# Kernel optimization log

Hardware: AMD Instinct MI355X
Metric: run time of the kernel (lower is better)

## Reference

```python
import jax, jax.numpy as jnp
import numpy as np

EPS = 1e-8  # EPSILON in original repo (sharpen denom); cosine eps matches torch default 1e-8
MAX_SHIFT = 1
M_FEAT = 128


def _lstm_cell(x, h, c, W_ih, W_hh, b_ih, b_hh):
    gates = x @ W_ih.T + b_ih + h @ W_hh.T + b_hh
    i, f, g, o = jnp.split(gates, 4, axis=1)
    c_new = jax.nn.sigmoid(f) * c + jax.nn.sigmoid(i) * jnp.tanh(g)
    h_new = jax.nn.sigmoid(o) * jnp.tanh(c_new)
    return h_new, c_new


def _content_address(bank, k, b):
    # torch cosine_similarity over dim 2: dot / max(|m||k|, eps)
    dot = jnp.einsum('bnm,bm->bn', bank, k)
    denom = jnp.maximum(jnp.linalg.norm(bank, axis=2) * jnp.linalg.norm(k, axis=1, keepdims=True), 1e-8)
    return jax.nn.softmax(b * dot / denom, axis=1)


def _shift(w, s):
    # circular unroll then valid cross-correlation with per-batch kernel s [B, 2*MAX_SHIFT+1]
    wp = jnp.concatenate([w[:, -MAX_SHIFT:], w, w[:, :MAX_SHIFT]], axis=1)
    N = w.shape[1]
    taps = 2 * MAX_SHIFT + 1
    return sum(s[:, i:i + 1] * wp[:, i:i + N] for i in range(taps))


def _sharpen(w, r):
    wr = w ** r
    return wr / (wr.sum(axis=1, keepdims=True) + EPS)


def _move(bank, w_prev, k, b, g, s, r):
    w = _content_address(bank, k, b)
    w = w + (1.0 - g) * w_prev  # faithful: w_c is NOT scaled by g in the source
    w = _shift(w, s)
    return _sharpen(w, r)


def _split_read(p):
    M = M_FEAT
    k = p[:, :M]
    b = jax.nn.softplus(p[:, M:M + 1])
    g = jax.nn.sigmoid(p[:, M + 1:M + 2])
    s = jax.nn.softmax(p[:, M + 2:M + 5], axis=1)
    r = 1.0 + jax.nn.softplus(p[:, M + 5:M + 6])
    return k, b, g, s, r


def _split_write(p):
    M = M_FEAT
    k, b, g, s, r = _split_read(p[:, :M + 6])
    e = jax.nn.sigmoid(p[:, M + 6:M + 6 + M])
    a = p[:, M + 6 + M:M + 6 + 2 * M]
    return k, b, g, s, r, e, a


def setup_inputs() -> dict:
    key = jax.random.key(0)
    ks = jax.random.split(key, 16)
    B, E, H, N, M, O = 64, 256, 512, 4096, 128, 256
    rd_out, wr_out = M + 2 * MAX_SHIFT + 4, 3 * M + 2 * MAX_SHIFT + 4
    sc = 0.05
    return {
        'x': jax.random.normal(ks[0], (B, E), jnp.float32),
        'h_prev': jax.random.normal(ks[1], (B, H), jnp.float32),
        'c_prev': jax.random.normal(ks[2], (B, H), jnp.float32),
        'bank': jax.random.normal(ks[3], (B, N, M), jnp.float32) * 0.1,
        'read_w_prev': jnp.zeros((3, B, N), jnp.float32),
        'write_w_prev': jnp.zeros((3, B, N), jnp.float32),
        'W_ih': jax.random.normal(ks[4], (4 * H, E), jnp.float32) * sc,
        'W_hh': jax.random.normal(ks[5], (4 * H, H), jnp.float32) * sc,
        'b_ih': jax.random.normal(ks[6], (4 * H,), jnp.float32) * sc,
        'b_hh': jax.random.normal(ks[7], (4 * H,), jnp.float32) * sc,
        'read_W': jax.random.normal(ks[8], (3, rd_out, H), jnp.float32) * sc,
        'read_b': jax.random.normal(ks[9], (3, rd_out), jnp.float32) * sc,
        'write_W': jax.random.normal(ks[10], (3, wr_out, H), jnp.float32) * sc,
        'write_b': jax.random.normal(ks[11], (3, wr_out), jnp.float32) * sc,
        'out_W': jax.random.normal(ks[12], (O, 3 * M + H), jnp.float32) * sc,
        'out_b': jax.random.normal(ks[13], (O,), jnp.float32) * sc,
    }


def reference(x, h_prev, c_prev, bank, read_w_prev, write_w_prev,
              W_ih, W_hh, b_ih, b_hh, read_W, read_b, write_W, write_b,
              out_W, out_b):
    h, c = _lstm_cell(x, h_prev, c_prev, W_ih, W_hh, b_ih, b_hh)
    reads = []
    for i in range(3):  # head_num=3, structurally distinct params per head
        # write head: update bank
        pw = h @ write_W[i].T + write_b[i]
        k, b, g, s, r, e, a = _split_write(pw)
        ww = _move(bank, write_w_prev[i], k, b, g, s, r)
        bank = bank * (1.0 - ww[:, :, None] * e[:, None, :]) + ww[:, :, None] * a[:, None, :]
        # read head: read from updated bank
        pr = h @ read_W[i].T + read_b[i]
        k, b, g, s, r = _split_read(pr)
        wr = _move(bank, read_w_prev[i], k, b, g, s, r)
        reads.append(jnp.einsum('bn,bnm->bm', wr, bank))
    out = jnp.concatenate(reads + [h], axis=1) @ out_W.T + out_b
    return out
```

## Files before the change

kernel.cpp:

```cpp
#include <hip/hip_runtime.h>
#include <math.h>

namespace {

constexpr int kB = 64;
constexpr int kN = 4096;
constexpr int kM = 128;
constexpr int kH = 512;
constexpr int kE = 256;
constexpr int kO = 256;
constexpr int kGates = 4 * kH;
constexpr int kCatW = 3 * kM + kH;
constexpr int kPRow = 1600;
constexpr int kWN = kB * kN;
constexpr float kLog2e = 1.4426950408889634f;

__device__ __forceinline__ float sigm_(float x) { return 1.f / (1.f + expf(-x)); }
__device__ __forceinline__ float softplus_(float x) { return x > 20.f ? x : log1pf(expf(x)); }

__global__ __launch_bounds__(256) void gates_gemm(const float* __restrict__ x,
                                                  const float* __restrict__ W_ih,
                                                  const float* __restrict__ h_prev,
                                                  const float* __restrict__ W_hh,
                                                  float* __restrict__ gates,
                                                  const float* __restrict__ out_b,
                                                  float* __restrict__ out,
                                                  float* __restrict__ cat) {
  if (blockIdx.x == 32) {
    const int tid = threadIdx.x;
    for (int i = tid; i < kB * kO; i += 256) out[i] = out_b[i & (kO - 1)];
    for (int i = tid; i < kB * 384; i += 256) cat[(i / 384) * kCatW + (i % 384)] = 0.f;
    return;
  }
  __shared__ float As[64][68];
  __shared__ float Ws[64][68];
  const int tid = threadIdx.x;
  const int j0 = blockIdx.x * 64;
  const int b0 = (tid & 15) * 4;
  const int j4 = (tid >> 4) * 4;
  float acc[4][4] = {};
  for (int kc = 0; kc < 12; kc++) {
    const bool isx = kc < 4;
    const float* A = isx ? x : h_prev;
    const float* W = isx ? W_ih : W_hh;
    const int lda = isx ? kE : kH;
    const int k0 = (isx ? kc : (kc - 4)) * 64;
    __syncthreads();
#pragma unroll
    for (int i = 0; i < 4; i++) {
      int idx = tid + i * 256;
      int bb = idx >> 4;
      int kk = (idx & 15) * 4;
      float4 v = *(const float4*)(A + (size_t)bb * lda + k0 + kk);
      As[kk][bb] = v.x; As[kk + 1][bb] = v.y; As[kk + 2][bb] = v.z; As[kk + 3][bb] = v.w;
      float4 w = *(const float4*)(W + (size_t)(j0 + bb) * lda + k0 + kk);
      Ws[kk][bb] = w.x; Ws[kk + 1][bb] = w.y; Ws[kk + 2][bb] = w.z; Ws[kk + 3][bb] = w.w;
    }
    __syncthreads();
#pragma unroll 2
    for (int k = 0; k < 64; k++) {
      float4 av = *(const float4*)&As[k][b0];
      float4 wv = *(const float4*)&Ws[k][j4];
      float aa[4] = {av.x, av.y, av.z, av.w};
      float ww[4] = {wv.x, wv.y, wv.z, wv.w};
#pragma unroll
      for (int ii = 0; ii < 4; ii++)
#pragma unroll
        for (int jj = 0; jj < 4; jj++) acc[ii][jj] += aa[ii] * ww[jj];
    }
  }
#pragma unroll
  for (int ii = 0; ii < 4; ii++) {
    float4 st = make_float4(acc[ii][0], acc[ii][1], acc[ii][2], acc[ii][3]);
    *(float4*)&gates[(size_t)(b0 + ii) * kGates + j0 + j4] = st;
  }
}

__global__ __launch_bounds__(256) void lstm_nl(const float* __restrict__ gates,
                                               const float* __restrict__ b_ih,
                                               const float* __restrict__ b_hh,
                                               const float* __restrict__ c_prev,
                                               float* __restrict__ cat) {
  int idx = blockIdx.x * 256 + threadIdx.x;
  if (idx >= kB * kH) return;
  int b = idx >> 9;
  int hh = idx & (kH - 1);
  const float* g = gates + (size_t)b * kGates;
  float i_ = g[hh]          + b_ih[hh]          + b_hh[hh];
  float f_ = g[kH + hh]     + b_ih[kH + hh]     + b_hh[kH + hh];
  float g_ = g[2 * kH + hh] + b_ih[2 * kH + hh] + b_hh[2 * kH + hh];
  float o_ = g[3 * kH + hh] + b_ih[3 * kH + hh] + b_hh[3 * kH + hh];
  float c = sigm_(f_) * c_prev[idx] + sigm_(i_) * tanhf(g_);
  cat[(size_t)b * kCatW + 3 * kM + hh] = sigm_(o_) * tanhf(c);
}

__global__ __launch_bounds__(256) void proj_gemm(const float* __restrict__ cat,
                                                 const float* __restrict__ write_W,
                                                 const float* __restrict__ read_W,
                                                 float* __restrict__ praw) {
  __shared__ float As[64][68];
  __shared__ float Ws[64][68];
  const float* A = cat + 3 * kM;
  const int tid = threadIdx.x;
  const int j0 = blockIdx.x * 64;
  const int b0 = (tid & 15) * 4;
  const int j4 = (tid >> 4) * 4;
  float acc[4][4] = {};
  for (int kc = 0; kc < 8; kc++) {
    const int k0 = kc * 64;
    __syncthreads();
#pragma unroll
    for (int i = 0; i < 4; i++) {
      int idx = tid + i * 256;
      int bb = idx >> 4;
      int kk = (idx & 15) * 4;
      float4 v = *(const float4*)(A + (size_t)bb * kCatW + k0 + kk);
      As[kk][bb] = v.x; As[kk + 1][bb] = v.y; As[kk + 2][bb] = v.z; As[kk + 3][bb] = v.w;
      int j = j0 + bb;
      float4 w = make_float4(0.f, 0.f, 0.f, 0.f);
      if (j < 1170)      w = *(const float4*)(write_W + (size_t)j * kH + k0 + kk);
      else if (j < 1572) w = *(const float4*)(read_W + (size_t)(j - 1170) * kH + k0 + kk);
      Ws[kk][bb] = w.x; Ws[kk + 1][bb] = w.y; Ws[kk + 2][bb] = w.z; Ws[kk + 3][bb] = w.w;
    }
    __syncthreads();
#pragma unroll 2
    for (int k = 0; k < 64; k++) {
      float4 av = *(const float4*)&As[k][b0];
      float4 wv = *(const float4*)&Ws[k][j4];
      float aa[4] = {av.x, av.y, av.z, av.w};
      float ww[4] = {wv.x, wv.y, wv.z, wv.w};
#pragma unroll
      for (int ii = 0; ii < 4; ii++)
#pragma unroll
        for (int jj = 0; jj < 4; jj++) acc[ii][jj] += aa[ii] * ww[jj];
    }
  }
  if (j0 + j4 < 1572) {
#pragma unroll
    for (int ii = 0; ii < 4; ii++) {
      float4 st = make_float4(acc[ii][0], acc[ii][1], acc[ii][2], acc[ii][3]);
      *(float4*)&praw[(size_t)(b0 + ii) * kPRow + j0 + j4] = st;
    }
  }
}

__global__ __launch_bounds__(128) void split_params(const float* __restrict__ praw,
                                                    const float* __restrict__ write_b,
                                                    const float* __restrict__ read_b,
                                                    float* __restrict__ kwb, float* __restrict__ krb,
                                                    float* __restrict__ evb, float* __restrict__ avb,
                                                    float* __restrict__ scal,
                                                    float* __restrict__ sdot) {
  const int b = blockIdx.x;
  const int m = threadIdx.x;
  __shared__ float red[2];
  for (int i = 0; i < 3; i++) {
    const float* p = praw + (size_t)b * kPRow + i * 390;
    const float* wb = write_b + i * 390;
    float kv = p[m] + wb[m];
    kwb[((size_t)i * kB + b) * kM + m] = kv;
    evb[((size_t)i * kB + b) * kM + m] = sigm_(p[134 + m] + wb[134 + m]);
    avb[((size_t)i * kB + b) * kM + m] = p[262 + m] + wb[262 + m];
    float sq = kv * kv;
#pragma unroll
    for (int mm = 1; mm < 64; mm <<= 1) sq += __shfl_xor(sq, mm, 64);
    __syncthreads();
    if ((m & 63) == 0) red[m >> 6] = sq;
    __syncthreads();
    if (m == 0) {
      float* s = scal + ((size_t)i * kB + b) * 8;
      s[0] = softplus_(p[128] + wb[128]);
      s[1] = sigm_(p[129] + wb[129]);
      s[2] = 1.f + softplus_(p[133] + wb[133]);
      float x0 = p[130] + wb[130], x1 = p[131] + wb[131], x2 = p[132] + wb[132];
      float mx = fmaxf(x0, fmaxf(x1, x2));
// ... 19 lines not shown
      float* s = scal + ((size_t)(3 + i) * kB + b) * 8;
      s[0] = softplus_(p[128] + rb[128]);
      s[1] = sigm_(p[129] + rb[129]);
      s[2] = 1.f + softplus_(p[133] + rb[133]);
      float x0 = p[130] + rb[130], x1 = p[131] + rb[131], x2 = p[132] + rb[132];
      float mx = fmaxf(x0, fmaxf(x1, x2));
      float e0 = expf(x0 - mx), e1 = expf(x1 - mx), e2 = expf(x2 - mx);
      float si = 1.f / (e0 + e1 + e2);
      s[3] = e0 * si; s[4] = e1 * si; s[5] = e2 * si;
      s[6] = sqrtf(red[0] + red[1]);
    }
    __syncthreads();
  }
  __syncthreads();
  if (m < 64) {
    const float* a0 = avb + ((size_t)0 * kB + b) * kM;
    const float* a2 = avb + ((size_t)2 * kB + b) * kM;
    const float* u[5] = {a0, a0, a0, a2, a2};
    const float* v[5] = {krb + ((size_t)0 * kB + b) * kM,
                         kwb + ((size_t)1 * kB + b) * kM,
                         a0,
                         krb + ((size_t)2 * kB + b) * kM,
                         a2};
#pragma unroll
    for (int d = 0; d < 5; d++) {
      float s = u[d][m] * v[d][m] + u[d][m + 64] * v[d][m + 64];
#pragma unroll
      for (int mm = 1; mm < 64; mm <<= 1) s += __shfl_xor(s, mm, 64);
      if (m == 0) sdot[b * 8 + d] = s;
    }
  }
}

__global__ __launch_bounds__(256, 4) void passA_k(const float* __restrict__ bank,
                                                  const float* __restrict__ kwb,
                                                  const float* __restrict__ krb,
                                                  const float* __restrict__ evb,
                                                  const float* __restrict__ avb,
                                                  float* __restrict__ mA) {
  const int b = blockIdx.y, chunk = blockIdx.x;
  const int tid = threadIdx.x;
  const int lane = tid & 63, wv = tid >> 6, sub = lane >> 4, lm = lane & 15;
  const int m8 = lm * 8;
  float kw0r[8], kr0r[8], kw1r[8], a0r[8], e0r[8];
#pragma unroll
  for (int t = 0; t < 8; t++) {
    kw0r[t] = kwb[((size_t)0 * kB + b) * kM + m8 + t];
    kr0r[t] = krb[((size_t)0 * kB + b) * kM + m8 + t];
    kw1r[t] = kwb[((size_t)1 * kB + b) * kM + m8 + t];
    a0r[t]  = avb[((size_t)0 * kB + b) * kM + m8 + t];
    e0r[t]  = evb[((size_t)0 * kB + b) * kM + m8 + t];
  }
  const size_t bbase = (size_t)b * kN * kM;
  const size_t brow = (size_t)b * kN;
  const int row0 = chunk * 256 + wv * 4 + sub;
  const float* rp = bank + bbase + (size_t)row0 * kM + m8;
  float4 c0 = *(const float4*)rp;
  float4 c1 = *(const float4*)(rp + 4);
  for (int it = 0; it < 16; it++) {
    float v[8] = {c0.x, c0.y, c0.z, c0.w, c1.x, c1.y, c1.z, c1.w};
    if (it < 15) {
      const float* np = bank + bbase + (size_t)(row0 + (it + 1) * 16) * kM + m8;
      c0 = *(const float4*)np;
      c1 = *(const float4*)(np + 4);
    }
    const int row = row0 + it * 16;
    float s[10] = {};
#pragma unroll
    for (int t = 0; t < 8; t++) {
      float be = v[t] * e0r[t];
      s[0] += v[t] * kw0r[t];
      s[1] += v[t] * v[t];
      s[2] += v[t] * kr0r[t];
      s[3] += be * kr0r[t];
      s[4] += v[t] * kw1r[t];
      s[5] += be * kw1r[t];
      s[6] += be * v[t];
      s[7] += be * be;
      s[8] += v[t] * a0r[t];
      s[9] += be * a0r[t];
    }
#pragma unroll
    for (int m = 1; m < 16; m <<= 1)
#pragma unroll
      for (int k = 0; k < 10; k++) s[k] += __shfl_xor(s[k], m, 64);
    if (lm == 0) {
#pragma unroll
      for (int k = 0; k < 10; k++) mA[(size_t)k * kWN + brow + row] = s[k];
    }
  }
}

__device__ void addr_core4(int tid, float* loc, const float* sc, const float* __restrict__ wp,
                           float* wb, float* red) {
  const float g = sc[1], r = sc[2];
  const float s0 = sc[3], s1c = sc[4], s2 = sc[5];
  const int lane = tid & 63, wid = tid >> 6;
  __syncthreads();
  float mx = fmaxf(fmaxf(loc[0], loc[1]), fmaxf(loc[2], loc[3]));
#pragma unroll
  for (int m = 1; m < 64; m <<= 1) mx = fmaxf(mx, __shfl_xor(mx, m, 64));
  if (lane == 0) red[wid] = mx;
  __syncthreads();
  mx = red[0];
#pragma unroll
  for (int k = 1; k < 16; k++) mx = fmaxf(mx, red[k]);
  float sum = 0.f;
#pragma unroll
  for (int i = 0; i < 4; i++) { loc[i] = exp2f((loc[i] - mx) * kLog2e); sum += loc[i]; }
#pragma unroll
  for (int m = 1; m < 64; m <<= 1) sum += __shfl_xor(sum, m, 64);
  __syncthreads();
  if (lane == 0) red[wid] = sum;
  __syncthreads();
  sum = red[0];
#pragma unroll
  for (int k = 1; k < 16; k++) sum += red[k];
  const float inv = 1.f / sum;
  const float omg = 1.f - g;
#pragma unroll
  for (int i = 0; i < 4; i++) {
    int n = tid + i * 1024;
    wb[n] = loc[i] * inv + omg * wp[n];
  }
  __syncthreads();
  float ssum = 0.f;
#pragma unroll
  for (int i = 0; i < 4; i++) {
    int n = tid + i * 1024;
    float sh = s0 * wb[(n + kN - 1) & (kN - 1)] + s1c * wb[n] + s2 * wb[(n + 1) & (kN - 1)];
    float y = (sh > 0.f) ? exp2f(r * log2f(sh)) : 0.f;
    loc[i] = y;
    ssum += y;
  }
#pragma unroll
  for (int m = 1; m < 64; m <<= 1) ssum += __shfl_xor(ssum, m, 64);
  __syncthreads();
  if (lane == 0) red[wid] = ssum;
  __syncthreads();
  ssum = red[0];
#pragma unroll
  for (int k = 1; k < 16; k++) ssum += red[k];
  const float invs = 1.f / (ssum + 1e-8f);
#pragma unroll
  for (int i = 0; i < 4; i++) loc[i] *= invs;
  __syncthreads();
}

__global__ __launch_bounds__(1024) void a12_k(const float* __restrict__ mA,
                                              const float* __restrict__ scal,
                                              const float* __restrict__ sdot,
                                              const float* __restrict__ read_w_prev,
                                              const float* __restrict__ write_w_prev,
                                              float* __restrict__ wwv,
                                              float* __restrict__ wrv) {
  const int b = blockIdx.x;
  const int tid = threadIdx.x;
  __shared__ float wb[kN];
  __shared__ float red[16];
  const size_t brow = (size_t)b * kN;
  float loc[4], w0r[4], q1r[4];
  {
    const float* sc = scal + ((size_t)0 * kB + b) * 8;
    const float beta = sc[0], kn = sc[6];
#pragma unroll
    for (int i = 0; i < 4; i++) {
      size_t idx = brow + tid + i * 1024;
      float d = mA[0 * (size_t)kWN + idx];
      float q = mA[1 * (size_t)kWN + idx];
      loc[i] = beta * d / fmaxf(sqrtf(fmaxf(q, 0.f)) * kn, 1e-8f);
    }
    addr_core4(tid, loc, sc, write_w_prev + brow, wb, red);
#pragma unroll
    for (int i = 0; i < 4; i++) { wwv[brow + tid + i * 1024] = loc[i]; w0r[i] = loc[i]; }
  }
  {
    const float* sc = scal + ((size_t)3 * kB + b) * 8;
    const float beta = sc[0], kn = sc[6];
    const float sa0kr0 = sdot[b * 8 + 0], sa0a0 = sdot[b * 8 + 2];
#pragma unroll
    for (int i = 0; i < 4; i++) {
      size_t idx = brow + tid + i * 1024;
      float w0 = w0r[i], w0q = w0 * w0;
      float q1 = mA[1 * (size_t)kWN + idx]
               - 2.f * w0 * mA[6 * (size_t)kWN + idx]
               + w0q * mA[7 * (size_t)kWN + idx]
               + 2.f * w0 * mA[8 * (size_t)kWN + idx]
               - 2.f * w0q * mA[9 * (size_t)kWN + idx]
               + w0q * sa0a0;
      q1r[i] = q1;
      float d = mA[2 * (size_t)kWN + idx] - w0 * mA[3 * (size_t)kWN + idx] + w0 * sa0kr0;
      loc[i] = beta * d / fmaxf(sqrtf(fmaxf(q1, 0.f)) * kn, 1e-8f);
    }
    addr_core4(tid, loc, sc, read_w_prev + brow, wb, red);
#pragma unroll
    for (int i = 0; i < 4; i++) wrv[brow + tid + i * 1024] = loc[i];
  }
  {
    const float* sc = scal + ((size_t)1 * kB + b) * 8;
    const float beta = sc[0], kn = sc[6];
    const float sa0kw1 = sdot[b * 8 + 1];
#pragma unroll
    for (int i = 0; i < 4; i++) {
      size_t idx = brow + tid + i * 1024;
      float w0 = w0r[i];
      float d = mA[4 * (size_t)kWN + idx] - w0 * mA[5 * (size_t)kWN + idx] + w0 * sa0kw1;
      loc[i] = beta * d / fmaxf(sqrtf(fmaxf(q1r[i], 0.f)) * kn, 1e-8f);
    }
    addr_core4(tid, loc, sc, write_w_prev + kWN + brow, wb, red);
#pragma unroll
    for (int i = 0; i < 4; i++) wwv[kWN + brow + tid + i * 1024] = loc[i];
  }
}

__global__ __launch_bounds__(256, 4) void passB_k(const float* __restrict__ bank,
                                                  const float* __restrict__ wwv,
                                                  const float* __restrict__ wrv,
                                                  const float* __restrict__ kwb,
                                                  const float* __restrict__ krb,
                                                  const float* __restrict__ evb,
                                                  const float* __restrict__ avb,
                                                  float* __restrict__ cat,
                                                  float* __restrict__ mB) {
  const int b = blockIdx.y, chunk = blockIdx.x;
  const int tid = threadIdx.x;
  const int lane = tid & 63, wv = tid >> 6, sub = lane >> 4, lm = lane & 15;
  const int m8 = lm * 8;
  float e0r[8], a0r[8], e1r[8], a1r[8], kr1r[8], kw2r[8], kr2r[8], e2r[8], a2r[8];
#pragma unroll
  for (int t = 0; t < 8; t++) {
    e0r[t]  = evb[((size_t)0 * kB + b) * kM + m8 + t];
    a0r[t]  = avb[((size_t)0 * kB + b) * kM + m8 + t];
    e1r[t]  = evb[((size_t)1 * kB + b) * kM + m8 + t];
    a1r[t]  = avb[((size_t)1 * kB + b) * kM + m8 + t];
    kr1r[t] = krb[((size_t)1 * kB + b) * kM + m8 + t];
    kw2r[t] = kwb[((size_t)2 * kB + b) * kM + m8 + t];
    kr2r[t] = krb[((size_t)2 * kB + b) * kM + m8 + t];
    e2r[t]  = evb[((size_t)2 * kB + b) * kM + m8 + t];
    a2r[t]  = avb[((size_t)2 * kB + b) * kM + m8 + t];
  }
  float racc[8] = {};
  __shared__ float rlds[kM];
  if (tid < kM) rlds[tid] = 0.f;
  const size_t bbase = (size_t)b * kN * kM;
  const size_t brow = (size_t)b * kN;
  const int row0 = chunk * 256 + wv * 4 + sub;
  const float* rp = bank + bbase + (size_t)row0 * kM + m8;
  float4 c0 = *(const float4*)rp;
  float4 c1 = *(const float4*)(rp + 4);
  float w0p = wwv[brow + row0];
  float w1p = wwv[kWN + brow + row0];
  float wr0p = wrv[brow + row0];
  for (int it = 0; it < 16; it++) {
    float v[8] = {c0.x, c0.y, c0.z, c0.w, c1.x, c1.y, c1.z, c1.w};
    const float w0 = w0p, w1 = w1p, wr0 = wr0p;
    if (it < 15) {
      const int nrow = row0 + (it + 1) * 16;
      const float* np = bank + bbase + (size_t)nrow * kM + m8;
      c0 = *(const float4*)np;
      c1 = *(const float4*)(np + 4);
      w0p = wwv[brow + nrow];
      w1p = wwv[kWN + brow + nrow];
      wr0p = wrv[brow + nrow];
    }
    const int row = row0 + it * 16;
#pragma unroll
    for (int t = 0; t < 8; t++) {
      v[t] += w0 * (a0r[t] - e0r[t] * v[t]);
      racc[t] += wr0 * v[t];
      v[t] += w1 * (a1r[t] - e1r[t] * v[t]);
    }
    float s[9] = {};
#pragma unroll
    for (int t = 0; t < 8; t++) {
      float ve = v[t] * e2r[t];
      s[0] += v[t] * kr1r[t];
      s[1] += v[t] * kw2r[t];
      s[2] += v[t] * v[t];
      s[3] += v[t] * kr2r[t];
      s[4] += ve * kr2r[t];
      s[5] += ve * v[t];
      s[6] += ve * ve;
      s[7] += v[t] * a2r[t];
      s[8] += ve * a2r[t];
    }
#pragma unroll
    for (int m = 1; m < 16; m <<= 1)
#pragma unroll
      for (int k = 0; k < 9; k++) s[k] += __shfl_xor(s[k], m, 64);
    if (lm == 0) {
#pragma unroll
      for (int k = 0; k < 9; k++) mB[(size_t)k * kWN + brow + row] = s[k];
    }
  }
  __syncthreads();
#pragma unroll
  for (int t = 0; t < 8; t++) {
    racc[t] += __shfl_xor(racc[t], 16, 64);
    racc[t] += __shfl_xor(racc[t], 32, 64);
  }
  if (sub == 0) {
#pragma unroll
    for (int t = 0; t < 8; t++) atomicAdd(&rlds[m8 + t], racc[t]);
  }
  __syncthreads();
  if (tid < kM) atomicAdd(&cat[(size_t)b * kCatW + tid], rlds[tid]);
}

__global__ __launch_bounds__(1024) void a34_k(const float* __restrict__ mB,
                                              const float* __restrict__ scal,
                                              const float* __restrict__ sdot,
                                              const float* __restrict__ read_w_prev,
                                              const float* __restrict__ write_w_prev,
                                              float* __restrict__ wwv,
                                              float* __restrict__ wrv) {
  const int b = blockIdx.x;
  const int tid = threadIdx.x;
  __shared__ float wb[kN];
  __shared__ float red[16];
  const size_t brow = (size_t)b * kN;
  float loc[4], w2r[4];
  {
    const float* sc = scal + ((size_t)4 * kB + b) * 8;
    const float beta = sc[0], kn = sc[6];
#pragma unroll
    for (int i = 0; i < 4; i++) {
      size_t idx = brow + tid + i * 1024;
      float d = mB[0 * (size_t)kWN + idx];
      float q = mB[2 * (size_t)kWN + idx];
      loc[i] = beta * d / fmaxf(sqrtf(fmaxf(q, 0.f)) * kn, 1e-8f);
    }
    addr_core4(tid, loc, sc, read_w_prev + kWN + brow, wb, red);
#pragma unroll
    for (int i = 0; i < 4; i++) wrv[kWN + brow + tid + i * 1024] = loc[i];
  }
  {
    const float* sc = scal + ((size_t)2 * kB + b) * 8;
    const float beta = sc[0], kn = sc[6];
#pragma unroll
    for (int i = 0; i < 4; i++) {
      size_t idx = brow + tid + i * 1024;
      float d = mB[1 * (size_t)kWN + idx];
      float q = mB[2 * (size_t)kWN + idx];
      loc[i] = beta * d / fmaxf(sqrtf(fmaxf(q, 0.f)) * kn, 1e-8f);
    }
    addr_core4(tid, loc, sc, write_w_prev + 2 * kWN + brow, wb, red);
#pragma unroll
    for (int i = 0; i < 4; i++) { wwv[2 * (size_t)kWN + brow + tid + i * 1024] = loc[i]; w2r[i] = loc[i]; }
  }
  {
    const float* sc = scal + ((size_t)5 * kB + b) * 8;
    const float beta = sc[0], kn = sc[6];
    const float sa2kr2 = sdot[b * 8 + 3], sa2a2 = sdot[b * 8 + 4];
#pragma unroll
    for (int i = 0; i < 4; i++) {
      size_t idx = brow + tid + i * 1024;
      float w2 = w2r[i], w2q = w2 * w2;
      float q3 = mB[2 * (size_t)kWN + idx]
               - 2.f * w2 * mB[5 * (size_t)kWN + idx]
               + w2q * mB[6 * (size_t)kWN + idx]
               + 2.f * w2 * mB[7 * (size_t)kWN + idx]
               - 2.f * w2q * mB[8 * (size_t)kWN + idx]
               + w2q * sa2a2;
      float d = mB[3 * (size_t)kWN + idx] - w2 * mB[4 * (size_t)kWN + idx] + w2 * sa2kr2;
      loc[i] = beta * d / fmaxf(sqrtf(fmaxf(q3, 0.f)) * kn, 1e-8f);
    }
    addr_core4(tid, loc, sc, read_w_prev + 2 * kWN + brow, wb, red);
#pragma unroll
    for (int i = 0; i < 4; i++) wrv[2 * (size_t)kWN + brow + tid + i * 1024] = loc[i];
  }
}

__global__ __launch_bounds__(256, 4) void passC_k(const float* __restrict__ bank,
                                                  const float* __restrict__ wwv,
                                                  const float* __restrict__ wrv,
                                                  const float* __restrict__ evb,
                                                  const float* __restrict__ avb,
                                                  float* __restrict__ cat) {
  const int b = blockIdx.y, chunk = blockIdx.x;
  const int tid = threadIdx.x;
  const int lane = tid & 63, wv = tid >> 6, sub = lane >> 4, lm = lane & 15;
  const int m8 = lm * 8;
  float e_r[3][8], a_r[3][8];
#pragma unroll
  for (int j = 0; j < 3; j++)
#pragma unroll
    for (int t = 0; t < 8; t++) {
      e_r[j][t] = evb[((size_t)j * kB + b) * kM + m8 + t];
      a_r[j][t] = avb[((size_t)j * kB + b) * kM + m8 + t];
    }
  float racc1[8] = {}, racc2[8] = {};
  __shared__ float rlds[2][kM];
  if (tid < kM) { rlds[0][tid] = 0.f; rlds[1][tid] = 0.f; }
  const size_t bbase = (size_t)b * kN * kM;
  const size_t brow = (size_t)b * kN;
  const int row0 = chunk * 256 + wv * 4 + sub;
  const float* rp = bank + bbase + (size_t)row0 * kM + m8;
  float4 c0 = *(const float4*)rp;
  float4 c1 = *(const float4*)(rp + 4);
  float w0p = wwv[brow + row0];
  float w1p = wwv[kWN + brow + row0];
  float w2p = wwv[2 * (size_t)kWN + brow + row0];
  float wr1p = wrv[kWN + brow + row0];
  float wr2p = wrv[2 * (size_t)kWN + brow + row0];
  for (int it = 0; it < 16; it++) {
    float v[8] = {c0.x, c0.y, c0.z, c0.w, c1.x, c1.y, c1.z, c1.w};
    const float w0 = w0p, w1 = w1p, w2 = w2p, wr1 = wr1p, wr2 = wr2p;
    if (it < 15) {
      const int nrow = row0 + (it + 1) * 16;
      const float* np = bank + bbase + (size_t)nrow * kM + m8;
      c0 = *(const float4*)np;
      c1 = *(const float4*)(np + 4);
      w0p = wwv[brow + nrow];
      w1p = wwv[kWN + brow + nrow];
      w2p = wwv[2 * (size_t)kWN + brow + nrow];
      wr1p = wrv[kWN + brow + nrow];
      wr2p = wrv[2 * (size_t)kWN + brow + nrow];
    }
#pragma unroll
    for (int t = 0; t < 8; t++) {
      v[t] += w0 * (a_r[0][t] - e_r[0][t] * v[t]);
      v[t] += w1 * (a_r[1][t] - e_r[1][t] * v[t]);
      racc1[t] += wr1 * v[t];
      v[t] += w2 * (a_r[2][t] - e_r[2][t] * v[t]);
      racc2[t] += wr2 * v[t];
    }
  }
  __syncthreads();
#pragma unroll
  for (int t = 0; t < 8; t++) {
    racc1[t] += __shfl_xor(racc1[t], 16, 64);
    racc1[t] += __shfl_xor(racc1[t], 32, 64);
    racc2[t] += __shfl_xor(racc2[t], 16, 64);
    racc2[t] += __shfl_xor(racc2[t], 32, 64);
  }
  if (sub == 0) {
#pragma unroll
    for (int t = 0; t < 8; t++) {
      atomicAdd(&rlds[0][m8 + t], racc1[t]);
      atomicAdd(&rlds[1][m8 + t], racc2[t]);
    }
  }
  __syncthreads();
  if (tid < kM) {
    atomicAdd(&cat[(size_t)b * kCatW + kM + tid], rlds[0][tid]);
    atomicAdd(&cat[(size_t)b * kCatW + 2 * kM + tid], rlds[1][tid]);
  }
}

__global__ __launch_bounds__(256) void out_gemm(const float* __restrict__ A,
// ... 42 lines not shown
}

extern "C" void kernel_launch(void* const* d_in, const int* in_sizes, int n_in,
                              void* d_out, int out_size, void* d_ws, size_t ws_size,
                              hipStream_t stream) {
  const float* x            = (const float*)d_in[0];
  const float* h_prev       = (const float*)d_in[1];
  const float* c_prev       = (const float*)d_in[2];
  const float* bank         = (const float*)d_in[3];
  const float* read_w_prev  = (const float*)d_in[4];
  const float* write_w_prev = (const float*)d_in[5];
  const float* W_ih         = (const float*)d_in[6];
  const float* W_hh         = (const float*)d_in[7];
  const float* b_ih         = (const float*)d_in[8];
  const float* b_hh         = (const float*)d_in[9];
  const float* read_W       = (const float*)d_in[10];
  const float* read_b       = (const float*)d_in[11];
  const float* write_W      = (const float*)d_in[12];
  const float* write_b      = (const float*)d_in[13];
  const float* out_W        = (const float*)d_in[14];
  const float* out_b        = (const float*)d_in[15];
  float* out = (float*)d_out;

  float* ws    = (float*)d_ws;
  float* gates = ws;
  float* praw  = gates + kB * kGates;
  float* cat   = praw + kB * kPRow;
  float* kwb   = cat + kB * kCatW;
  float* krb   = kwb + 3 * kB * kM;
  float* evb   = krb + 3 * kB * kM;
  float* avb   = evb + 3 * kB * kM;
  float* scal  = avb + 3 * kB * kM;
  float* sdot  = scal + 6 * kB * 8;
  float* wwv   = sdot + kB * 8;
  float* wrv   = wwv + 3 * kWN;
  float* mA    = wrv + 3 * kWN;
  float* mB    = mA + 10 * (size_t)kWN;

  gates_gemm<<<33, 256, 0, stream>>>(x, W_ih, h_prev, W_hh, gates, out_b, out, cat);
  lstm_nl<<<(kB * kH) / 256, 256, 0, stream>>>(gates, b_ih, b_hh, c_prev, cat);
  proj_gemm<<<25, 256, 0, stream>>>(cat, write_W, read_W, praw);
  split_params<<<64, 128, 0, stream>>>(praw, write_b, read_b, kwb, krb, evb, avb, scal, sdot);

  passA_k<<<dim3(16, kB), 256, 0, stream>>>(bank, kwb, krb, evb, avb, mA);
  a12_k<<<64, 1024, 0, stream>>>(mA, scal, sdot, read_w_prev, write_w_prev, wwv, wrv);
  passB_k<<<dim3(16, kB), 256, 0, stream>>>(bank, wwv, wrv, kwb, krb, evb, avb, cat, mB);
  a34_k<<<64, 1024, 0, stream>>>(mB, scal, sdot, read_w_prev, write_w_prev, wwv, wrv);
  passC_k<<<dim3(16, kB), 256, 0, stream>>>(bank, wwv, wrv, evb, avb, cat);
  out_gemm<<<dim3(kO / 64, kCatW / 128), 256, 0, stream>>>(cat, out_W, out);

  (void)in_sizes; (void)n_in; (void)out_size; (void)ws_size;
}
```

Baseline: 445.2 us.

## Retile small GEMMs, fuse LSTM into projection, pack head weights, double-buffer bank loads

The gates GEMM is retiled across 128 blocks so it uses more CUs, and the LSTM nonlinearity is fused into the projection GEMM, now spread over 200 blocks with h recomputed per block. Per-row weight vectors and pass statistics move from planar arrays to interleaved records (8 and 12 floats) so each row is fetched with a few vector loads. The bank-streaming passes switch to two-deep register prefetch, and the occupancy hint is dropped from their launch bounds. These changes target launch count, under-filled grids and scattered small loads, at the cost of redundant LSTM work and higher register pressure.

```diff
diff --git a/kernel.cpp b/kernel.cpp
--- a/kernel.cpp
+++ b/kernel.cpp
@@ -26,19 +26,20 @@
                                                   const float* __restrict__ out_b,
                                                   float* __restrict__ out,
                                                   float* __restrict__ cat) {
-  if (blockIdx.x == 32) {
+  if (blockIdx.x == 128) {
     const int tid = threadIdx.x;
     for (int i = tid; i < kB * kO; i += 256) out[i] = out_b[i & (kO - 1)];
     for (int i = tid; i < kB * 384; i += 256) cat[(i / 384) * kCatW + (i % 384)] = 0.f;
     return;
   }
-  __shared__ float As[64][68];
-  __shared__ float Ws[64][68];
+  __shared__ float At[64 * 20];
+  __shared__ float Wt[64 * 65];
   const int tid = threadIdx.x;
-  const int j0 = blockIdx.x * 64;
-  const int b0 = (tid & 15) * 4;
-  const int j4 = (tid >> 4) * 4;
-  float acc[4][4] = {};
+  const int b0 = (blockIdx.x >> 5) * 16;
+  const int j0 = (blockIdx.x & 31) * 64;
+  const int jg = tid & 63;
+  const int bq4 = (tid >> 6) * 4;
+  float acc[4] = {};
   for (int kc = 0; kc < 12; kc++) {
     const bool isx = kc < 4;
     const float* A = isx ? x : h_prev;
@@ -46,101 +47,92 @@
     const int lda = isx ? kE : kH;
     const int k0 = (isx ? kc : (kc - 4)) * 64;
     __syncthreads();
+    {
+      int bb = tid >> 4;
+      int kk = (tid & 15) * 4;
+      float4 v = *(const float4*)(A + (size_t)(b0 + bb) * lda + k0 + kk);
+      At[(kk + 0) * 20 + bb] = v.x; At[(kk + 1) * 20 + bb] = v.y;
+      At[(kk + 2) * 20 + bb] = v.z; At[(kk + 3) * 20 + bb] = v.w;
+    }
 #pragma unroll
     for (int i = 0; i < 4; i++) {
       int idx = tid + i * 256;
-      int bb = idx >> 4;
+      int jj = idx >> 4;
       int kk = (idx & 15) * 4;
-      float4 v = *(const float4*)(A + (size_t)bb * lda + k0 + kk);
-      As[kk][bb] = v.x; As[kk + 1][bb] = v.y; As[kk + 2][bb] = v.z; As[kk + 3][bb] = v.w;
-      float4 w = *(const float4*)(W + (size_t)(j0 + bb) * lda + k0 + kk);
-      Ws[kk][bb] = w.x; Ws[kk + 1][bb] = w.y; Ws[kk + 2][bb] = w.z; Ws[kk + 3][bb] = w.w;
-    }
-    __syncthreads();
-#pragma unroll 2
+      float4 w = *(const float4*)(W + (size_t)(j0 + jj) * lda + k0 + kk);
+      Wt[(kk + 0) * 65 + jj] = w.x; Wt[(kk + 1) * 65 + jj] = w.y;
+      Wt[(kk + 2) * 65 + jj] = w.z; Wt[(kk + 3) * 65 + jj] = w.w;
+    }
+    __syncthreads();
+#pragma unroll 4
     for (int k = 0; k < 64; k++) {
-      float4 av = *(const float4*)&As[k][b0];
-      float4 wv = *(const float4*)&Ws[k][j4];
-      float aa[4] = {av.x, av.y, av.z, av.w};
-      float ww[4] = {wv.x, wv.y, wv.z, wv.w};
-#pragma unroll
-      for (int ii = 0; ii < 4; ii++)
-#pragma unroll
-        for (int jj = 0; jj < 4; jj++) acc[ii][jj] += aa[ii] * ww[jj];
-    }
-  }
-#pragma unroll
-  for (int ii = 0; ii < 4; ii++) {
-    float4 st = make_float4(acc[ii][0], acc[ii][1], acc[ii][2], acc[ii][3]);
-    *(float4*)&gates[(size_t)(b0 + ii) * kGates + j0 + j4] = st;
-  }
-}
-
-__global__ __launch_bounds__(256) void lstm_nl(const float* __restrict__ gates,
-                                               const float* __restrict__ b_ih,
-                                               const float* __restrict__ b_hh,
-                                               const float* __restrict__ c_prev,
-                                               float* __restrict__ cat) {
-  int idx = blockIdx.x * 256 + threadIdx.x;
-  if (idx >= kB * kH) return;
-  int b = idx >> 9;
-  int hh = idx & (kH - 1);
-  const float* g = gates + (size_t)b * kGates;
-  float i_ = g[hh]          + b_ih[hh]          + b_hh[hh];
-  float f_ = g[kH + hh]     + b_ih[kH + hh]     + b_hh[kH + hh];
-  float g_ = g[2 * kH + hh] + b_ih[2 * kH + hh] + b_hh[2 * kH + hh];
-  float o_ = g[3 * kH + hh] + b_ih[3 * kH + hh] + b_hh[3 * kH + hh];
-  float c = sigm_(f_) * c_prev[idx] + sigm_(i_) * tanhf(g_);
-  cat[(size_t)b * kCatW + 3 * kM + hh] = sigm_(o_) * tanhf(c);
-}
-
-__global__ __launch_bounds__(256) void proj_gemm(const float* __restrict__ cat,
+      float4 av = *(const float4*)&At[k * 20 + bq4];
+      float wv = Wt[k * 65 + jg];
+      acc[0] += av.x * wv; acc[1] += av.y * wv; acc[2] += av.z * wv; acc[3] += av.w * wv;
+    }
+  }
+#pragma unroll
+  for (int i = 0; i < 4; i++)
+    gates[(size_t)(b0 + bq4 + i) * kGates + j0 + jg] = acc[i];
+}
+
+__global__ __launch_bounds__(256) void proj_gemm(const float* __restrict__ gates,
+                                                 const float* __restrict__ b_ih,
+                                                 const float* __restrict__ b_hh,
+                                                 const float* __restrict__ c_prev,
                                                  const float* __restrict__ write_W,
                                                  const float* __restrict__ read_W,
-                                                 float* __restrict__ praw) {
-  __shared__ float As[64][68];
-  __shared__ float Ws[64][68];
-  const float* A = cat + 3 * kM;
+                                                 float* __restrict__ praw,
+                                                 float* __restrict__ cat) {
+  __shared__ float hs[512 * 12];
+  __shared__ float Wt[64 * 65];
   const int tid = threadIdx.x;
-  const int j0 = blockIdx.x * 64;
-  const int b0 = (tid & 15) * 4;
-  const int j4 = (tid >> 4) * 4;
-  float acc[4][4] = {};
+  const int bs = blockIdx.x / 25;
+  const int jt = blockIdx.x % 25;
+  const int b0 = bs * 8;
+  const int j0 = jt * 64;
+  for (int i = tid; i < 8 * 512; i += 256) {
+    int bb = i >> 9, kk = i & 511;
+    int b = b0 + bb;
+    const float* g = gates + (size_t)b * kGates;
+    float i_ = g[kk]           + b_ih[kk]           + b_hh[kk];
+    float f_ = g[512 + kk]     + b_ih[512 + kk]     + b_hh[512 + kk];
+    float g_ = g[1024 + kk]    + b_ih[1024 + kk]    + b_hh[1024 + kk];
+    float o_ = g[1536 + kk]    + b_ih[1536 + kk]    + b_hh[1536 + kk];
+    float c = sigm_(f_) * c_prev[(size_t)b * kH + kk] + sigm_(i_) * tanhf(g_);
+    float h = sigm_(o_) * tanhf(c);
+    hs[kk * 12 + bb] = h;
+    if (jt == 0) cat[(size_t)b * kCatW + 3 * kM + kk] = h;
+  }
+  const int jg = tid & 63;
+  const int bq2 = (tid >> 6) * 2;
+  float acc[2] = {};
   for (int kc = 0; kc < 8; kc++) {
     const int k0 = kc * 64;
     __syncthreads();
 #pragma unroll
     for (int i = 0; i < 4; i++) {
       int idx = tid + i * 256;
-      int bb = idx >> 4;
+      int jj = idx >> 4;
       int kk = (idx & 15) * 4;
-      float4 v = *(const float4*)(A + (size_t)bb * kCatW + k0 + kk);
-      As[kk][bb] = v.x; As[kk + 1][bb] = v.y; As[kk + 2][bb] = v.z; As[kk + 3][bb] = v.w;
-      int j = j0 + bb;
+      int j = j0 + jj;
       float4 w = make_float4(0.f, 0.f, 0.f, 0.f);
       if (j < 1170)      w = *(const float4*)(write_W + (size_t)j * kH + k0 + kk);
       else if (j < 1572) w = *(const float4*)(read_W + (size_t)(j - 1170) * kH + k0 + kk);
-      Ws[kk][bb] = w.x; Ws[kk + 1][bb] = w.y; Ws[kk + 2][bb] = w.z; Ws[kk + 3][bb] = w.w;
-    }
-    __syncthreads();
-#pragma unroll 2
+      Wt[(kk + 0) * 65 + jj] = w.x; Wt[(kk + 1) * 65 + jj] = w.y;
+      Wt[(kk + 2) * 65 + jj] = w.z; Wt[(kk + 3) * 65 + jj] = w.w;
+    }
+    __syncthreads();
+#pragma unroll 4
     for (int k = 0; k < 64; k++) {
-      float4 av = *(const float4*)&As[k][b0];
-      float4 wv = *(const float4*)&Ws[k][j4];
-      float aa[4] = {av.x, av.y, av.z, av.w};
-      float ww[4] = {wv.x, wv.y, wv.z, wv.w};
-#pragma unroll
-      for (int ii = 0; ii < 4; ii++)
-#pragma unroll
-        for (int jj = 0; jj < 4; jj++) acc[ii][jj] += aa[ii] * ww[jj];
-    }
-  }
-  if (j0 + j4 < 1572) {
-#pragma unroll
-    for (int ii = 0; ii < 4; ii++) {
-      float4 st = make_float4(acc[ii][0], acc[ii][1], acc[ii][2], acc[ii][3]);
-      *(float4*)&praw[(size_t)(b0 + ii) * kPRow + j0 + j4] = st;
-    }
+      float2 av = *(const float2*)&hs[(k0 + k) * 12 + bq2];
+      float wv = Wt[k * 65 + jg];
+      acc[0] += av.x * wv; acc[1] += av.y * wv;
+    }
+  }
+  if (j0 + jg < 1572) {
+    praw[(size_t)(b0 + bq2 + 0) * kPRow + j0 + jg] = acc[0];
+    praw[(size_t)(b0 + bq2 + 1) * kPRow + j0 + jg] = acc[1];
   }
 }
 
@@ -226,12 +218,12 @@
   }
 }
 
-__global__ __launch_bounds__(256, 4) void passA_k(const float* __restrict__ bank,
-                                                  const float* __restrict__ kwb,
-                                                  const float* __restrict__ krb,
-                                                  const float* __restrict__ evb,
-                                                  const float* __restrict__ avb,
-                                                  float* __restrict__ mA) {
+__global__ __launch_bounds__(256) void passA_k(const float* __restrict__ bank,
+                                               const float* __restrict__ kwb,
+                                               const float* __restrict__ krb,
+                                               const float* __restrict__ evb,
+                                               const float* __restrict__ avb,
+                                               float* __restrict__ mA) {
   const int b = blockIdx.y, chunk = blockIdx.x;
   const int tid = threadIdx.x;
   const int lane = tid & 63, wv = tid >> 6, sub = lane >> 4, lm = lane & 15;
@@ -248,15 +240,25 @@
   const size_t bbase = (size_t)b * kN * kM;
   const size_t brow = (size_t)b * kN;
   const int row0 = chunk * 256 + wv * 4 + sub;
-  const float* rp = bank + bbase + (size_t)row0 * kM + m8;
-  float4 c0 = *(const float4*)rp;
-  float4 c1 = *(const float4*)(rp + 4);
+  const float* base = bank + bbase + (size_t)row0 * kM + m8;
+  float4 pA0 = *(const float4*)(base);
+  float4 pA1 = *(const float4*)(base + 4);
+  float4 pB0 = *(const float4*)(base + (size_t)16 * kM);
+  float4 pB1 = *(const float4*)(base + (size_t)16 * kM + 4);
   for (int it = 0; it < 16; it++) {
-    float v[8] = {c0.x, c0.y, c0.z, c0.w, c1.x, c1.y, c1.z, c1.w};
-    if (it < 15) {
-      const float* np = bank + bbase + (size_t)(row0 + (it + 1) * 16) * kM + m8;
-      c0 = *(const float4*)np;
-      c1 = *(const float4*)(np + 4);
+    float v[8];
+    if ((it & 1) == 0) {
+      v[0]=pA0.x; v[1]=pA0.y; v[2]=pA0.z; v[3]=pA0.w; v[4]=pA1.x; v[5]=pA1.y; v[6]=pA1.z; v[7]=pA1.w;
+      if (it + 2 < 16) {
+        const float* np = base + (size_t)(it + 2) * 16 * kM;
+        pA0 = *(const float4*)np; pA1 = *(const float4*)(np + 4);
+      }
+    } else {
+      v[0]=pB0.x; v[1]=pB0.y; v[2]=pB0.z; v[3]=pB0.w; v[4]=pB1.x; v[5]=pB1.y; v[6]=pB1.z; v[7]=pB1.w;
+      if (it + 2 < 16) {
+        const float* np = base + (size_t)(it + 2) * 16 * kM;
+        pB0 = *(const float4*)np; pB1 = *(const float4*)(np + 4);
+      }
     }
     const int row = row0 + it * 16;
     float s[10] = {};
@@ -279,8 +281,10 @@
 #pragma unroll
       for (int k = 0; k < 10; k++) s[k] += __shfl_xor(s[k], m, 64);
     if (lm == 0) {
-#pragma unroll
-      for (int k = 0; k < 10; k++) mA[(size_t)k * kWN + brow + row] = s[k];
+      float4* dst = (float4*)(mA + (size_t)(brow + row) * 12);
+      dst[0] = make_float4(s[0], s[1], s[2], s[3]);
+      dst[1] = make_float4(s[4], s[5], s[6], s[7]);
+      dst[2] = make_float4(s[8], s[9], 0.f, 0.f);
     }
   }
 }
@@ -346,8 +350,7 @@
                                               const float* __restrict__ sdot,
                                               const float* __restrict__ read_w_prev,
                                               const float* __restrict__ write_w_prev,
-                                              float* __restrict__ wwv,
-                                              float* __restrict__ wrv) {
+                                              float* __restrict__ wpack) {
   const int b = blockIdx.x;
   const int tid = threadIdx.x;
   __shared__ float wb[kN];
@@ -359,14 +362,16 @@
     const float beta = sc[0], kn = sc[6];
 #pragma unroll
     for (int i = 0; i < 4; i++) {
-      size_t idx = brow + tid + i * 1024;
-      float d = mA[0 * (size_t)kWN + idx];
-      float q = mA[1 * (size_t)kWN + idx];
-      loc[i] = beta * d / fmaxf(sqrtf(fmaxf(q, 0.f)) * kn, 1e-8f);
+      const float* mp = mA + (size_t)(brow + tid + i * 1024) * 12;
+      float4 q0 = *(const float4*)mp;
+      loc[i] = beta * q0.x / fmaxf(sqrtf(fmaxf(q0.y, 0.f)) * kn, 1e-8f);
     }
     addr_core4(tid, loc, sc, write_w_prev + brow, wb, red);
 #pragma unroll
-    for (int i = 0; i < 4; i++) { wwv[brow + tid + i * 1024] = loc[i]; w0r[i] = loc[i]; }
+    for (int i = 0; i < 4; i++) {
+      wpack[(size_t)(brow + tid + i * 1024) * 8 + 0] = loc[i];
+      w0r[i] = loc[i];
+    }
   }
   {
     const float* sc = scal + ((size_t)3 * kB + b) * 8;
@@ -374,21 +379,25 @@
     const float sa0kr0 = sdot[b * 8 + 0], sa0a0 = sdot[b * 8 + 2];
 #pragma unroll
     for (int i = 0; i < 4; i++) {
-      size_t idx = brow + tid + i * 1024;
+      const float* mp = mA + (size_t)(brow + tid + i * 1024) * 12;
+      float4 q0 = *(const float4*)mp;
+      float4 q1 = *(const float4*)(mp + 4);
+      float4 q2 = *(const float4*)(mp + 8);
       float w0 = w0r[i], w0q = w0 * w0;
-      float q1 = mA[1 * (size_t)kWN + idx]
-               - 2.f * w0 * mA[6 * (size_t)kWN + idx]
-               + w0q * mA[7 * (size_t)kWN + idx]
-               + 2.f * w0 * mA[8 * (size_t)kWN + idx]
-               - 2.f * w0q * mA[9 * (size_t)kWN + idx]
-               + w0q * sa0a0;
-      q1r[i] = q1;
-      float d = mA[2 * (size_t)kWN + idx] - w0 * mA[3 * (size_t)kWN + idx] + w0 * sa0kr0;
-      loc[i] = beta * d / fmaxf(sqrtf(fmaxf(q1, 0.f)) * kn, 1e-8f);
+      float q1v = q0.y
+                - 2.f * w0 * q1.z
+                + w0q * q1.w
+                + 2.f * w0 * q2.x
+                - 2.f * w0q * q2.y
+                + w0q * sa0a0;
+      q1r[i] = q1v;
+      float d = q0.z - w0 * q0.w + w0 * sa0kr0;
+      loc[i] = beta * d / fmaxf(sqrtf(fmaxf(q1v, 0.f)) * kn, 1e-8f);
     }
     addr_core4(tid, loc, sc, read_w_prev + brow, wb, red);
 #pragma unroll
-    for (int i = 0; i < 4; i++) wrv[brow + tid + i * 1024] = loc[i];
+    for (int i = 0; i < 4; i++)
+      wpack[(size_t)(brow + tid + i * 1024) * 8 + 2] = loc[i];
   }
   {
     const float* sc = scal + ((size_t)1 * kB + b) * 8;
@@ -396,26 +405,27 @@
     const float sa0kw1 = sdot[b * 8 + 1];
 #pragma unroll
     for (int i = 0; i < 4; i++) {
-      size_t idx = brow + tid + i * 1024;
+      const float* mp = mA + (size_t)(brow + tid + i * 1024) * 12;
+      float4 q1 = *(const float4*)(mp + 4);
       float w0 = w0r[i];
-      float d = mA[4 * (size_t)kWN + idx] - w0 * mA[5 * (size_t)kWN + idx] + w0 * sa0kw1;
+      float d = q1.x - w0 * q1.y + w0 * sa0kw1;
       loc[i] = beta * d / fmaxf(sqrtf(fmaxf(q1r[i], 0.f)) * kn, 1e-8f);
     }
     addr_core4(tid, loc, sc, write_w_prev + kWN + brow, wb, red);
 #pragma unroll
-    for (int i = 0; i < 4; i++) wwv[kWN + brow + tid + i * 1024] = loc[i];
-  }
-}
-
-__global__ __launch_bounds__(256, 4) void passB_k(const float* __restrict__ bank,
-                                                  const float* __restrict__ wwv,
-                                                  const float* __restrict__ wrv,
-                                                  const float* __restrict__ kwb,
-                                                  const float* __restrict__ krb,
-                                                  const float* __restrict__ evb,
-                                                  const float* __restrict__ avb,
-                                                  float* __restrict__ cat,
-                                                  float* __restrict__ mB) {
+    for (int i = 0; i < 4; i++)
+      wpack[(size_t)(brow + tid + i * 1024) * 8 + 1] = loc[i];
+  }
+}
+
+__global__ __launch_bounds__(256) void passB_k(const float* __restrict__ bank,
+                                               const float* __restrict__ wpack,
+                                               const float* __restrict__ kwb,
+                                               const float* __restrict__ krb,
+                                               const float* __restrict__ evb,
+                                               const float* __restrict__ avb,
+                                               float* __restrict__ cat,
+                                               float* __restrict__ mB) {
   const int b = blockIdx.y, chunk = blockIdx.x;
   const int tid = threadIdx.x;
   const int lane = tid & 63, wv = tid >> 6, sub = lane >> 4, lm = lane & 15;
@@ -439,23 +449,33 @@
   const size_t bbase = (size_t)b * kN * kM;
   const size_t brow = (size_t)b * kN;
   const int row0 = chunk * 256 + wv * 4 + sub;
-  const float* rp = bank + bbase + (size_t)row0 * kM + m8;
-  float4 c0 = *(const float4*)rp;
-  float4 c1 = *(const float4*)(rp + 4);
-  float w0p = wwv[brow + row0];
-  float w1p = wwv[kWN + brow + row0];
-  float wr0p = wrv[brow + row0];
+  const float* base = bank + bbase + (size_t)row0 * kM + m8;
+  const float* wbase = wpack + (size_t)(brow + row0) * 8;
+  float4 pA0 = *(const float4*)(base);
+  float4 pA1 = *(const float4*)(base + 4);
+  float4 wA  = *(const float4*)(wbase);
+  float4 pB0 = *(const float4*)(base + (size_t)16 * kM);
+  float4 pB1 = *(const float4*)(base + (size_t)16 * kM + 4);
+  float4 wB  = *(const float4*)(wbase + (size_t)16 * 8);
   for (int it = 0; it < 16; it++) {
-    float v[8] = {c0.x, c0.y, c0.z, c0.w, c1.x, c1.y, c1.z, c1.w};
-    const float w0 = w0p, w1 = w1p, wr0 = wr0p;
-    if (it < 15) {
-      const int nrow = row0 + (it + 1) * 16;
-      const float* np = bank + bbase + (size_t)nrow * kM + m8;
-      c0 = *(const float4*)np;
-      c1 = *(const float4*)(np + 4);
-      w0p = wwv[brow + nrow];
-      w1p = wwv[kWN + brow + nrow];
-      wr0p = wrv[brow + nrow];
+    float v[8];
+    float w0, w1, wr0;
+    if ((it & 1) == 0) {
+      v[0]=pA0.x; v[1]=pA0.y; v[2]=pA0.z; v[3]=pA0.w; v[4]=pA1.x; v[5]=pA1.y; v[6]=pA1.z; v[7]=pA1.w;
+      w0 = wA.x; w1 = wA.y; wr0 = wA.z;
+      if (it + 2 < 16) {
+        const float* np = base + (size_t)(it + 2) * 16 * kM;
+        pA0 = *(const float4*)np; pA1 = *(const float4*)(np + 4);
+        wA = *(const float4*)(wbase + (size_t)(it + 2) * 16 * 8);
+      }
+    } else {
+      v[0]=pB0.x; v[1]=pB0.y; v[2]=pB0.z; v[3]=pB0.w; v[4]=pB1.x; v[5]=pB1.y; v[6]=pB1.z; v[7]=pB1.w;
+      w0 = wB.x; w1 = wB.y; wr0 = wB.z;
+      if (it + 2 < 16) {
+        const float* np = base + (size_t)(it + 2) * 16 * kM;
+        pB0 = *(const float4*)np; pB1 = *(const float4*)(np + 4);
+        wB = *(const float4*)(wbase + (size_t)(it + 2) * 16 * 8);
+      }
     }
     const int row = row0 + it * 16;
 #pragma unroll
@@ -483,8 +503,10 @@
 #pragma unroll
       for (int k = 0; k < 9; k++) s[k] += __shfl_xor(s[k], m, 64);
     if (lm == 0) {
-#pragma unroll
-      for (int k = 0; k < 9; k++) mB[(size_t)k * kWN + brow + row] = s[k];
+      float4* dst = (float4*)(mB + (size_t)(brow + row) * 12);
+      dst[0] = make_float4(s[0], s[1], s[2], s[3]);
+      dst[1] = make_float4(s[4], s[5], s[6], s[7]);
+      dst[2] = make_float4(s[8], 0.f, 0.f, 0.f);
     }
   }
   __syncthreads();
@@ -506,8 +528,7 @@
                                               const float* __restrict__ sdot,
                                               const float* __restrict__ read_w_prev,
                                               const float* __restrict__ write_w_prev,
-                                              float* __restrict__ wwv,
-                                              float* __restrict__ wrv) {
+                                              float* __restrict__ wpack) {
   const int b = blockIdx.x;
   const int tid = threadIdx.x;
   __shared__ float wb[kN];
@@ -519,28 +540,30 @@
     const float beta = sc[0], kn = sc[6];
 #pragma unroll
     for (int i = 0; i < 4; i++) {
-      size_t idx = brow + tid + i * 1024;
-      float d = mB[0 * (size_t)kWN + idx];
-      float q = mB[2 * (size_t)kWN + idx];
-      loc[i] = beta * d / fmaxf(sqrtf(fmaxf(q, 0.f)) * kn, 1e-8f);
+      const float* mp = mB + (size_t)(brow + tid + i * 1024) * 12;
+      float4 q0 = *(const float4*)mp;
+      loc[i] = beta * q0.x / fmaxf(sqrtf(fmaxf(q0.z, 0.f)) * kn, 1e-8f);
     }
     addr_core4(tid, loc, sc, read_w_prev + kWN + brow, wb, red);
 #pragma unroll
-    for (int i = 0; i < 4; i++) wrv[kWN + brow + tid + i * 1024] = loc[i];
+    for (int i = 0; i < 4; i++)
+      wpack[(size_t)(brow + tid + i * 1024) * 8 + 4] = loc[i];
   }
   {
     const float* sc = scal + ((size_t)2 * kB + b) * 8;
     const float beta = sc[0], kn = sc[6];
 #pragma unroll
     for (int i = 0; i < 4; i++) {
-      size_t idx = brow + tid + i * 1024;
-      float d = mB[1 * (size_t)kWN + idx];
-      float q = mB[2 * (size_t)kWN + idx];
-      loc[i] = beta * d / fmaxf(sqrtf(fmaxf(q, 0.f)) * kn, 1e-8f);
+      const float* mp = mB + (size_t)(brow + tid + i * 1024) * 12;
+      float4 q0 = *(const float4*)mp;
+      loc[i] = beta * q0.y / fmaxf(sqrtf(fmaxf(q0.z, 0.f)) * kn, 1e-8f);
     }
     addr_core4(tid, loc, sc, write_w_prev + 2 * kWN + brow, wb, red);
 #pragma unroll
-    for (int i = 0; i < 4; i++) { wwv[2 * (size_t)kWN + brow + tid + i * 1024] = loc[i]; w2r[i] = loc[i]; }
+    for (int i = 0; i < 4; i++) {
+      wpack[(size_t)(brow + tid + i * 1024) * 8 + 3] = loc[i];
+      w2r[i] = loc[i];
+    }
   }
   {
     const float* sc = scal + ((size_t)5 * kB + b) * 8;
@@ -548,29 +571,32 @@
     const float sa2kr2 = sdot[b * 8 + 3], sa2a2 = sdot[b * 8 + 4];
 #pragma unroll
     for (int i = 0; i < 4; i++) {
-      size_t idx = brow + tid + i * 1024;
+      const float* mp = mB + (size_t)(brow + tid + i * 1024) * 12;
+      float4 q0 = *(const float4*)mp;
+      float4 q1 = *(const float4*)(mp + 4);
+      float4 q2 = *(const float4*)(mp + 8);
       float w2 = w2r[i], w2q = w2 * w2;
-      float q3 = mB[2 * (size_t)kWN + idx]
-               - 2.f * w2 * mB[5 * (size_t)kWN + idx]
-               + w2q * mB[6 * (size_t)kWN + idx]
-               + 2.f * w2 * mB[7 * (size_t)kWN + idx]
-               - 2.f * w2q * mB[8 * (size_t)kWN + idx]
+      float q3 = q0.z
+               - 2.f * w2 * q1.y
+               + w2q * q1.z
+               + 2.f * w2 * q1.w
+               - 2.f * w2q * q2.x
                + w2q * sa2a2;
-      float d = mB[3 * (size_t)kWN + idx] - w2 * mB[4 * (size_t)kWN + idx] + w2 * sa2kr2;
+      float d = q0.w - w2 * q1.x + w2 * sa2kr2;
       loc[i] = beta * d / fmaxf(sqrtf(fmaxf(q3, 0.f)) * kn, 1e-8f);
     }
     addr_core4(tid, loc, sc, read_w_prev + 2 * kWN + brow, wb, red);
 #pragma unroll
-    for (int i = 0; i < 4; i++) wrv[2 * (size_t)kWN + brow + tid + i * 1024] = loc[i];
-  }
-}
-
-__global__ __launch_bounds__(256, 4) void passC_k(const float* __restrict__ bank,
-                                                  const float* __restrict__ wwv,
-                                                  const float* __restrict__ wrv,
-                                                  const float* __restrict__ evb,
-                                                  const float* __restrict__ avb,
-                                                  float* __restrict__ cat) {
+    for (int i = 0; i < 4; i++)
+      wpack[(size_t)(brow + tid + i * 1024) * 8 + 5] = loc[i];
+  }
+}
+
+__global__ __launch_bounds__(256) void passC_k(const float* __restrict__ bank,
+                                               const float* __restrict__ wpack,
+                                               const float* __restrict__ evb,
+                                               const float* __restrict__ avb,
+                                               float* __restrict__ cat) {
   const int b = blockIdx.y, chunk = blockIdx.x;
   const int tid = threadIdx.x;
   const int lane = tid & 63, wv = tid >> 6, sub = lane >> 4, lm = lane & 15;
@@ -589,27 +615,37 @@
   const size_t bbase = (size_t)b * kN * kM;
   const size_t brow = (size_t)b * kN;
   const int row0 = chunk * 256 + wv * 4 + sub;
-  const float* rp = bank + bbase + (size_t)row0 * kM + m8;
-  float4 c0 = *(const float4*)rp;
-  float4 c1 = *(const float4*)(rp + 4);
-  float w0p = wwv[brow + row0];
-  float w1p = wwv[kWN + brow + row0];
-  float w2p = wwv[2 * (size_t)kWN + brow + row0];
-  float wr1p = wrv[kWN + brow + row0];
-  float wr2p = wrv[2 * (size_t)kWN + brow + row0];
+  const float* base = bank + bbase + (size_t)row0 * kM + m8;
+  const float* wbase = wpack + (size_t)(brow + row0) * 8;
+  float4 pA0 = *(const float4*)(base);
+  float4 pA1 = *(const float4*)(base + 4);
+  float4 wAa = *(const float4*)(wbase);
+  float4 wAb = *(const float4*)(wbase + 4);
+  float4 pB0 = *(const float4*)(base + (size_t)16 * kM);
+  float4 pB1 = *(const float4*)(base + (size_t)16 * kM + 4);
+  float4 wBa = *(const float4*)(wbase + (size_t)16 * 8);
+  float4 wBb = *(const float4*)(wbase + (size_t)16 * 8 + 4);
   for (int it = 0; it < 16; it++) {
-    float v[8] = {c0.x, c0.y, c0.z, c0.w, c1.x, c1.y, c1.z, c1.w};
-    const float w0 = w0p, w1 = w1p, w2 = w2p, wr1 = wr1p, wr2 = wr2p;
-    if (it < 15) {
-      const int nrow = row0 + (it + 1) * 16;
-      const float* np = bank + bbase + (size_t)nrow * kM + m8;
-      c0 = *(const float4*)np;
-      c1 = *(const float4*)(np + 4);
-      w0p = wwv[brow + nrow];
-      w1p = wwv[kWN + brow + nrow];
-      w2p = wwv[2 * (size_t)kWN + brow + nrow];
-      wr1p = wrv[kWN + brow + nrow];
-      wr2p = wrv[2 * (size_t)kWN + brow + nrow];
+    float v[8];
+    float w0, w1, w2, wr1, wr2;
+    if ((it & 1) == 0) {
+      v[0]=pA0.x; v[1]=pA0.y; v[2]=pA0.z; v[3]=pA0.w; v[4]=pA1.x; v[5]=pA1.y; v[6]=pA1.z; v[7]=pA1.w;
+      w0 = wAa.x; w1 = wAa.y; w2 = wAa.w; wr1 = wAb.x; wr2 = wAb.y;
+      if (it + 2 < 16) {
+        const float* np = base + (size_t)(it + 2) * 16 * kM;
+        pA0 = *(const float4*)np; pA1 = *(const float4*)(np + 4);
+        const float* wp = wbase + (size_t)(it + 2) * 16 * 8;
+        wAa = *(const float4*)wp; wAb = *(const float4*)(wp + 4);
+      }
+    } else {
+      v[0]=pB0.x; v[1]=pB0.y; v[2]=pB0.z; v[3]=pB0.w; v[4]=pB1.x; v[5]=pB1.y; v[6]=pB1.z; v[7]=pB1.w;
+      w0 = wBa.x; w1 = wBa.y; w2 = wBa.w; wr1 = wBb.x; wr2 = wBb.y;
+      if (it + 2 < 16) {
+        const float* np = base + (size_t)(it + 2) * 16 * kM;
+        pB0 = *(const float4*)np; pB1 = *(const float4*)(np + 4);
+        const float* wp = wbase + (size_t)(it + 2) * 16 * 8;
+        wBa = *(const float4*)wp; wBb = *(const float4*)(wp + 4);
+      }
     }
 #pragma unroll
     for (int t = 0; t < 8; t++) {
@@ -718,21 +754,19 @@
   float* avb   = evb + 3 * kB * kM;
   float* scal  = avb + 3 * kB * kM;
   float* sdot  = scal + 6 * kB * 8;
-  float* wwv   = sdot + kB * 8;
-  float* wrv   = wwv + 3 * kWN;
-  float* mA    = wrv + 3 * kWN;
-  float* mB    = mA + 10 * (size_t)kWN;
-
-  gates_gemm<<<33, 256, 0, stream>>>(x, W_ih, h_prev, W_hh, gates, out_b, out, cat);
-  lstm_nl<<<(kB * kH) / 256, 256, 0, stream>>>(gates, b_ih, b_hh, c_prev, cat);
-  proj_gemm<<<25, 256, 0, stream>>>(cat, write_W, read_W, praw);
+  float* wpack = sdot + kB * 8;
+  float* mA    = wpack + (size_t)kWN * 8;
+  float* mB    = mA + (size_t)kWN * 12;
+
+  gates_gemm<<<129, 256, 0, stream>>>(x, W_ih, h_prev, W_hh, gates, out_b, out, cat);
+  proj_gemm<<<200, 256, 0, stream>>>(gates, b_ih, b_hh, c_prev, write_W, read_W, praw, cat);
   split_params<<<64, 128, 0, stream>>>(praw, write_b, read_b, kwb, krb, evb, avb, scal, sdot);
 
   passA_k<<<dim3(16, kB), 256, 0, stream>>>(bank, kwb, krb, evb, avb, mA);
-  a12_k<<<64, 1024, 0, stream>>>(mA, scal, sdot, read_w_prev, write_w_prev, wwv, wrv);
-  passB_k<<<dim3(16, kB), 256, 0, stream>>>(bank, wwv, wrv, kwb, krb, evb, avb, cat, mB);
-  a34_k<<<64, 1024, 0, stream>>>(mB, scal, sdot, read_w_prev, write_w_prev, wwv, wrv);
-  passC_k<<<dim3(16, kB), 256, 0, stream>>>(bank, wwv, wrv, evb, avb, cat);
+  a12_k<<<64, 1024, 0, stream>>>(mA, scal, sdot, read_w_prev, write_w_prev, wpack);
+  passB_k<<<dim3(16, kB), 256, 0, stream>>>(bank, wpack, kwb, krb, evb, avb, cat, mB);
+  a34_k<<<64, 1024, 0, stream>>>(mB, scal, sdot, read_w_prev, write_w_prev, wpack);
+  passC_k<<<dim3(16, kB), 256, 0, stream>>>(bank, wpack, evb, avb, cat);
   out_gemm<<<dim3(kO / 64, kCatW / 128), 256, 0, stream>>>(cat, out_W, out);
 
   (void)in_sizes; (void)n_in; (void)out_size; (void)ws_size;
```

Measured after the change: 436.0 us. 1.02x faster.
